# Optimization experiments

Measured on AMD Instinct MI355X. Metric: run time of the kernel, lower is better.

## Reference

```python
import jax, jax.numpy as jnp
import numpy as np

N_NODES = 100000
N_EDGES = 1000000
IN_F, HID_F, OUT_F = 128, 128, 16


def setup_inputs() -> dict:
    key = jax.random.key(0)
    ks = jax.random.split(key, 8)
    x = jax.random.normal(ks[0], (N_NODES, IN_F), dtype=jnp.float32)
    src = jax.random.randint(ks[1], (N_EDGES,), 0, N_NODES, dtype=jnp.int64)
    dst = jax.random.randint(ks[2], (N_EDGES,), 0, N_NODES, dtype=jnp.int64)
    s = 1.0 / np.sqrt(HID_F)
    W1 = jax.random.normal(ks[3], (IN_F, HID_F), dtype=jnp.float32) * s
    W2 = jax.random.normal(ks[4], (HID_F, HID_F), dtype=jnp.float32) * s
    W3 = jax.random.normal(ks[5], (HID_F, HID_F), dtype=jnp.float32) * s
    W4 = jax.random.normal(ks[6], (HID_F, HID_F), dtype=jnp.float32) * s
    W5 = jax.random.normal(ks[7], (HID_F, OUT_F), dtype=jnp.float32) * s
    return {
        "x": x, "src": src, "dst": dst,
        "W1": W1, "b1": jnp.zeros((HID_F,), jnp.float32),
        "W2": W2, "b2": jnp.zeros((HID_F,), jnp.float32),
        "W3": W3, "b3": jnp.zeros((HID_F,), jnp.float32),
        "W4": W4, "b4": jnp.zeros((HID_F,), jnp.float32),
        "W5": W5, "b5": jnp.zeros((OUT_F,), jnp.float32),
    }


def reference(x, src, dst, W1, b1, W2, b2, W3, b3, W4, b4, W5, b5):
    N = x.shape[0]
    # in-degree per destination node (static graph, computed once)
    deg = jax.ops.segment_sum(jnp.ones_like(dst, dtype=x.dtype), dst, num_segments=N)
    inv = (1.0 / (deg + 1.0))[:, None]  # gcn aggregator normalizer: 1/(deg_in+1)

    def sage_gcn(h, W, b):
        # h_neigh[v] = (h[v] + sum_{u->v} h[u]) / (deg_in(v)+1); then linear
        agg = (h + jax.ops.segment_sum(h[src], dst, num_segments=N)) * inv
        return agg @ W + b

    h = jax.nn.relu(sage_gcn(x, W1, b1))
    h = jax.nn.relu(sage_gcn(h, W2, b2))
    h = jax.nn.relu(sage_gcn(h, W3, b3))
    h = jax.nn.relu(sage_gcn(h, W4, b4))
    h = sage_gcn(h, W5, b5)
    return jax.nn.log_softmax(h, axis=-1)
```

## Files before the change

### kernel.cpp

```cpp
#include <hip/hip_runtime.h>
#include <hip/hip_bf16.h>

#define NNODES 100000
#define NP (NNODES + 8)
#define NEDGES 1000000
#define HID 128
#define OUTF 16
#define NB 16
#define BCAP 81920
#define KB 64
#define BZT 1024
#define DBINS 32

typedef __attribute__((ext_vector_type(8))) short short8;
typedef __attribute__((ext_vector_type(4))) float floatx4;
typedef __attribute__((ext_vector_type(4))) unsigned int uintx4;
typedef unsigned int uint32;
typedef unsigned long long ull;
typedef unsigned short ushort16;

__device__ __forceinline__ float blo(uint32 u) { return __uint_as_float(u << 16); }
__device__ __forceinline__ float bhi(uint32 u) { return __uint_as_float(u & 0xffff0000u); }
__device__ __forceinline__ ushort16 f2b(float f) {
    __hip_bfloat16 h = __float2bfloat16(f);
    return *reinterpret_cast<ushort16*>(&h);
}
__device__ __forceinline__ uint32 pack2(float a, float b) {
    return (uint32)f2b(a) | ((uint32)f2b(b) << 16);
}


__global__ __launch_bounds__(BZT) void bucketize(const int* __restrict__ src,
                                                 const int* __restrict__ dst,
                                                 int* __restrict__ counts,
                                                 int* __restrict__ bcursor,
                                                 ull* __restrict__ stage, int E) {
    __shared__ int cnt[NB], lbase[NB], gbase[NB];
    __shared__ int2 buf[BZT];
    __shared__ unsigned char bb[BZT];
    int t = threadIdx.x;
    int e0 = blockIdx.x * BZT;
    int e = e0 + t;
    if (t < NB) cnt[t] = 0;
    __syncthreads();
    int s = 0; unsigned y = 0; int b = 0, r = 0;
    bool valid = e < E;
    if (valid) {
        s = src[e];
        int d = dst[e];
        int rk = atomicAdd(&counts[d], 1);
        y = (unsigned)d | ((unsigned)rk << 17);
        b = (int)((unsigned)d * NB / NNODES);
        r = atomicAdd(&cnt[b], 1);
    }
    __syncthreads();
    if (t == 0) {
        int run = 0;
        for (int i = 0; i < NB; i++) { lbase[i] = run; run += cnt[i]; }
    }
    __syncthreads();
    if (valid) {
        int p = lbase[b] + r;
        buf[p] = make_int2(s, (int)y);
        bb[p] = (unsigned char)b;
    }
    if (t < NB) gbase[t] = atomicAdd(&bcursor[t], cnt[t]);
    __syncthreads();
    int nvalid = min(BZT, E - e0);
    if (t < nvalid) {
        int b2 = bb[t];
        int2 sd = buf[t];
        int pos = gbase[b2] + (t - lbase[b2]);
        if (pos < BCAP) {
            ull val = (ull)(unsigned)sd.x | ((ull)(unsigned)sd.y << 32);
            __builtin_nontemporal_store(val, &stage[(size_t)b2 * BCAP + pos]);
        }
    }
}

__global__ __launch_bounds__(256) void fill2(const ull* __restrict__ stage,
                                             const int* __restrict__ bcursor,
                                             const int* __restrict__ offs,
                                             int* __restrict__ csr) {
    int blk = blockIdx.x;
    int b = (blk & 7) + 8 * ((blk >> 3) & 1);
    int slot = blk >> 4;
    int cntb = min(bcursor[b], BCAP);
    int per = (cntb + KB - 1) / KB;
    int s0 = slot * per;
    int s1 = min(s0 + per, cntb);
    const ull* st = stage + (size_t)b * BCAP;
    for (int i = s0 + threadIdx.x; i < s1; i += 256) {
        ull v = __builtin_nontemporal_load(&st[i]);
        int s = (int)(v & 0xffffffffu);
        unsigned y = (unsigned)(v >> 32);
        int d = (int)(y & 0x1ffffu);
        int r = (int)(y >> 17);
        csr[offs[d] + r] = s;
    }
}

__global__ void scan1(const int* __restrict__ counts, int* __restrict__ offs,
                      int* __restrict__ bsum, int N) {
    __shared__ int tmp[256];
    int t = threadIdx.x;
    int i = blockIdx.x * 256 + t;
    int v = (i < N) ? ((counts[i] + 7) & ~7) : 0;
    tmp[t] = v;
    __syncthreads();
    for (int d = 1; d < 256; d <<= 1) {
        int add = (t >= d) ? tmp[t - d] : 0;
        __syncthreads();
        tmp[t] += add;
        __syncthreads();
    }
    if (i < N) offs[i] = tmp[t] - v;
    if (t == 255) bsum[blockIdx.x] = tmp[255];
}

__global__ void scan2(int* __restrict__ bsum, int nb) {
    __shared__ int tmp[512];
    int t = threadIdx.x;
    int v = (t < nb) ? bsum[t] : 0;
    tmp[t] = v;
    __syncthreads();
    for (int d = 1; d < 512; d <<= 1) {
        int add = (t >= d) ? tmp[t - d] : 0;
        __syncthreads();
        tmp[t] += add;
        __syncthreads();
    }
    if (t < nb) bsum[t] = tmp[t] - v;
}

__global__ void scan3(int* __restrict__ offs, const int* __restrict__ bsum,
                      const int* __restrict__ counts, float* __restrict__ inv,
                      int N) {
    int i = blockIdx.x * 256 + threadIdx.x;
    if (i < N) {
        offs[i] += bsum[blockIdx.x];
        inv[i] = 1.0f / (float)(counts[i] + 1);
    }
}


__global__ __launch_bounds__(256) void binhist(const int* __restrict__ counts,
                                               int* __restrict__ bins, int N) {
    __shared__ int h[DBINS];
    int t = threadIdx.x;
    if (t < DBINS) h[t] = 0;
    __syncthreads();
    int i = blockIdx.x * 256 + t;
    if (i < N) {
        int bin = min((counts[i] + 7) >> 3, DBINS - 1);
        atomicAdd(&h[bin], 1);
    }
    __syncthreads();
    if (t < DBINS && h[t] > 0) atomicAdd(&bins[t], h[t]);
}

__global__ void binscan(int* __restrict__ bins) {
    if (threadIdx.x == 0) {
        int run = 0;
        for (int i = 0; i < DBINS; i++) {
            int c = bins[i];
            bins[i] = run;
            run += c;
        }
    }
}

__global__ __launch_bounds__(256) void dsort2(const int* __restrict__ counts,
                                              const int* __restrict__ offs,
                                              const float* __restrict__ inv,
                                              int* __restrict__ bins,
                                              int* __restrict__ begs, int* __restrict__ cnts,
                                              float* __restrict__ invs, int* __restrict__ outid,
                                              int* __restrict__ csr, int N) {
    __shared__ int h[DBINS], lbase[DBINS];
    int t = threadIdx.x;
    int i = blockIdx.x * 256 + t;
    if (t < DBINS) h[t] = 0;
    __syncthreads();
    int c = 0, bin = 0, r = 0;
    bool valid = i < N;
    if (valid) {
        c = counts[i];
        bin = min((c + 7) >> 3, DBINS - 1);
        r = atomicAdd(&h[bin], 1);
    }
    __syncthreads();
    if (t < DBINS) lbase[t] = (h[t] > 0) ? atomicAdd(&bins[t], h[t]) : 0;
    __syncthreads();
    if (valid) {
        int p = lbase[bin] + r;
        int o = offs[i];
        begs[p] = o;
        cnts[p] = c;
        invs[p] = inv[i];
        outid[p] = i;
        int c8 = (c + 7) & ~7;
        for (int k = c; k < c8; k++) csr[o + k] = NNODES;
    }
}

__global__ void zeropad(uint32* __restrict__ zb, uint32* __restrict__ hb,
                        uint32* __restrict__ z16b) {
    int t = threadIdx.x;
    for (int i = t; i < 512; i += 256) {
        int s = i >> 6, r = (i >> 3) & 7, k = i & 7;
        zb[((size_t)s * NP + NNODES + r) * 8 + k] = 0;
        hb[((size_t)s * NP + NNODES + r) * 8 + k] = 0;
    }
    if (t < 64) z16b[(size_t)(NNODES + (t >> 3)) * 8 + (t & 7)] = 0;
}


__global__ void pack_w(const float* __restrict__ W, ushort16* __restrict__ Wp) {
    int b = blockIdx.x;
    int lane = threadIdx.x;
    int nt = b >> 2, ks = b & 3;
    int n = nt * 16 + (lane & 15);
    int kbase = ks * 32 + ((lane >> 4) << 3);
    ushort16 tmp[8];
#pragma unroll
    for (int i = 0; i < 8; i++) tmp[i] = f2b(W[(size_t)(kbase + i) * HID + n]);
    *(uint4*)&Wp[((size_t)b * 64 + lane) * 8] = *(uint4*)tmp;
}


template <int AF32>
__global__ __launch_bounds__(256) void gemm_mfma(const void* __restrict__ Av,
                                                 const ushort16* __restrict__ Wp,
                                                 ushort16* __restrict__ Z, int M) {
    __shared__ __align__(16) ushort16 Wl[32 * 64 * 8];
    int t = threadIdx.x;
    const uint4* wp4 = (const uint4*)Wp;
    uint4* wl4 = (uint4*)Wl;
#pragma unroll
    for (int p = 0; p < 8; p++) wl4[t + p * 256] = wp4[t + p * 256];
    __syncthreads();

    int wv = t >> 6, lane = t & 63;
    int row = blockIdx.x * 64 + wv * 16 + (lane & 15);
    int rowc = min(row, M - 1);
    int kb = (lane >> 4) << 3;

    short8 a[4];
    if (AF32) {
        const float* A = (const float*)Av;
#pragma unroll
        for (int ks = 0; ks < 4; ks++) {
            const float* p = A + (size_t)rowc * HID + ks * 32 + kb;
            floatx4 lo = *(const floatx4*)p;
            floatx4 hi = *(const floatx4*)(p + 4);
            union { short8 s; ushort16 u[8]; } cv;
            cv.u[0] = f2b(lo.x); cv.u[1] = f2b(lo.y); cv.u[2] = f2b(lo.z); cv.u[3] = f2b(lo.w);
            cv.u[4] = f2b(hi.x); cv.u[5] = f2b(hi.y); cv.u[6] = f2b(hi.z); cv.u[7] = f2b(hi.w);
            a[ks] = cv.s;
        }
    } else {
        const ushort16* A = (const ushort16*)Av;
        int sl = kb >> 4, soff = kb & 8;
#pragma unroll
        for (int ks = 0; ks < 4; ks++) {
            int slice = ks * 2 + sl;
            a[ks] = *(const short8*)(A + ((size_t)slice * NP + rowc) * 16 + soff);
        }
    }

    floatx4 acc[8];
#pragma unroll
    for (int nt = 0; nt < 8; nt++) acc[nt] = (floatx4){0.f, 0.f, 0.f, 0.f};

#pragma unroll
    for (int nt = 0; nt < 8; nt++) {
#pragma unroll
        for (int ks = 0; ks < 4; ks++) {
            short8 b = *(const short8*)&Wl[(size_t)(((nt << 2) | ks) * 64 + lane) * 8];
            acc[nt] = __builtin_amdgcn_mfma_f32_16x16x32_bf16(a[ks], b, acc[nt], 0, 0, 0);
        }
    }

    int orow = blockIdx.x * 64 + wv * 16 + ((lane >> 4) << 2);
    int col = lane & 15;
#pragma unroll
    for (int i = 0; i < 4; i++) {
        int r = orow + i;
        if (r < M) {
#pragma unroll
            for (int nt = 0; nt < 8; nt++)
                Z[((size_t)nt * NP + r) * 16 + col] = f2b(acc[nt][i]);
        }
    }
}


#define ACC4(g)                                        \
    {                                                  \
        acc0.x += blo((g).x); acc0.y += bhi((g).x);    \
        acc1.x += blo((g).y); acc1.y += bhi((g).y);    \
        acc2.x += blo((g).z); acc2.y += bhi((g).z);    \
        acc3.x += blo((g).w); acc3.y += bhi((g).w);    \
    }

__global__ __launch_bounds__(256) void agg_sliced(const uint32* __restrict__ Z,
                                                  const int* __restrict__ begs,
                                                  const int* __restrict__ cnts,
                                                  const int* __restrict__ csr,
                                                  const float* __restrict__ invs,
                                                  const int* __restrict__ outid,
                                                  const float* __restrict__ bias,
                                                  uint32* __restrict__ H, int N) {
    int s = blockIdx.x & 7;
    int chunk = blockIdx.x >> 3;
    int t = threadIdx.x;
    int l = t & 1;
    int p = chunk * 128 + (t >> 1);
    int pairbase = t & 62;
    bool act = p < N;
    int pc = act ? p : N - 1;
    const uint4* Zs = (const uint4*)(Z + (size_t)s * NP * 8);
    uint4* Hs = (uint4*)(H + (size_t)s * NP * 8);

    int beg = begs[pc];
    int cnt8 = (cnts[pc] + 7) & ~7;
    float sc = invs[pc];
    int ov = outid[pc];

    uint4 sv = Zs[(size_t)ov * 2 + l];
    float2 acc0 = make_float2(blo(sv.x), bhi(sv.x));
    float2 acc1 = make_float2(blo(sv.y), bhi(sv.y));
    float2 acc2 = make_float2(blo(sv.z), bhi(sv.z));
    float2 acc3 = make_float2(blo(sv.w), bhi(sv.w));

    for (int j = 0; j < cnt8; j += 8) {
        int4 iv = *(const int4*)&csr[beg + j + 4 * l];
        uint4 g[8];
#pragma unroll
        for (int q = 0; q < 8; q++) {
            int c = (q & 3) == 0 ? iv.x : (q & 3) == 1 ? iv.y : (q & 3) == 2 ? iv.z : iv.w;
            int u = __shfl(c, pairbase + (q >> 2), 64);
            g[q] = Zs[(size_t)u * 2 + l];
        }
#pragma unroll
        for (int q = 0; q < 8; q++) ACC4(g[q]);
    }

    const float* bp = bias + s * 16 + l * 8;
    floatx4 b01 = *(const floatx4*)bp;
    floatx4 b23 = *(const floatx4*)(bp + 4);
    uintx4 o;
    o.x = pack2(fmaxf(acc0.x * sc + b01.x, 0.f), fmaxf(acc0.y * sc + b01.y, 0.f));
    o.y = pack2(fmaxf(acc1.x * sc + b01.z, 0.f), fmaxf(acc1.y * sc + b01.w, 0.f));
    o.z = pack2(fmaxf(acc2.x * sc + b23.x, 0.f), fmaxf(acc2.y * sc + b23.y, 0.f));
    o.w = pack2(fmaxf(acc3.x * sc + b23.z, 0.f), fmaxf(acc3.y * sc + b23.w, 0.f));
    if (act) __builtin_nontemporal_store(o, (uintx4*)&Hs[(size_t)ov * 2 + l]);
}


__global__ __launch_bounds__(256) void gemm16(const uint32* __restrict__ A,
                                              const float* __restrict__ W5,
                                              uint32* __restrict__ Z16, int M) {
    __shared__ float Ws[HID * OUTF];
    int t = threadIdx.x;
    for (int i = t; i < HID * OUTF; i += 256) Ws[i] = W5[i];
    __syncthreads();
    int gid = blockIdx.x * 256 + t;
    int r = gid >> 3, cp = gid & 7;
    if (r >= M) return;
    float a0 = 0.f, a1 = 0.f;
#pragma unroll
    for (int s8 = 0; s8 < 8; s8++) {
        const uint32* ar = A + ((size_t)s8 * NP + r) * 8;
#pragma unroll
        for (int k = 0; k < 8; k++) {
            uint32 u = ar[k];
            float f0 = blo(u), f1 = bhi(u);
            a0 += f0 * Ws[(s8 * 16 + 2 * k) * OUTF + 2 * cp] +
                  f1 * Ws[(s8 * 16 + 2 * k + 1) * OUTF + 2 * cp];
            a1 += f0 * Ws[(s8 * 16 + 2 * k) * OUTF + 2 * cp + 1] +
                  f1 * Ws[(s8 * 16 + 2 * k + 1) * OUTF + 2 * cp + 1];
        }
    }
    Z16[(size_t)r * 8 + cp] = pack2(a0, a1);
}


__global__ __launch_bounds__(256) void agg16_lsm(const uint32* __restrict__ Z16,
                                                 const int* __restrict__ offs,
                                                 const int* __restrict__ counts,
                                                 const int* __restrict__ csr,
                                                 const float* __restrict__ inv,
                                                 const float* __restrict__ b5,
                                                 float* __restrict__ out, int N) {
    int t = threadIdx.x;
    int l = t & 1;
    int v = blockIdx.x * 128 + (t >> 1);
    int pairbase = t & 62;
    bool act = v < N;
    int vc = act ? v : N - 1;
    const uint4* Zs = (const uint4*)Z16;

    uint4 sv = Zs[(size_t)vc * 2 + l];
    float2 acc0 = make_float2(blo(sv.x), bhi(sv.x));
    float2 acc1 = make_float2(blo(sv.y), bhi(sv.y));
    float2 acc2 = make_float2(blo(sv.z), bhi(sv.z));
    float2 acc3 = make_float2(blo(sv.w), bhi(sv.w));

    int beg = offs[vc];
    int cnt8 = (counts[vc] + 7) & ~7;
    for (int j = 0; j < cnt8; j += 8) {
        int4 iv = *(const int4*)&csr[beg + j + 4 * l];
        uint4 g[8];
#pragma unroll
        for (int q = 0; q < 8; q++) {
            int c = (q & 3) == 0 ? iv.x : (q & 3) == 1 ? iv.y : (q & 3) == 2 ? iv.z : iv.w;
            int u = __shfl(c, pairbase + (q >> 2), 64);
            g[q] = Zs[(size_t)u * 2 + l];
        }
#pragma unroll
        for (int q = 0; q < 8; q++) ACC4(g[q]);
    }

    float sc = inv[vc];
    const float* bp = b5 + l * 8;
    floatx4 b01 = *(const floatx4*)bp;
    floatx4 b23 = *(const floatx4*)(bp + 4);
    float val[8];
    val[0] = acc0.x * sc + b01.x; val[1] = acc0.y * sc + b01.y;
    val[2] = acc1.x * sc + b01.z; val[3] = acc1.y * sc + b01.w;
    val[4] = acc2.x * sc + b23.x; val[5] = acc2.y * sc + b23.y;
    val[6] = acc3.x * sc + b23.z; val[7] = acc3.y * sc + b23.w;
    float mm = val[0];
#pragma unroll
    for (int k = 1; k < 8; k++) mm = fmaxf(mm, val[k]);
    mm = fmaxf(mm, __shfl_xor(mm, 1, 64));
    float ss = 0.f;
#pragma unroll
    for (int k = 0; k < 8; k++) ss += expf(val[k] - mm);
    ss += __shfl_xor(ss, 1, 64);
    float ls = mm + logf(ss);
    if (act) {
        float4 o0 = make_float4(val[0] - ls, val[1] - ls, val[2] - ls, val[3] - ls);
        float4 o1 = make_float4(val[4] - ls, val[5] - ls, val[6] - ls, val[7] - ls);
        float* op = out + (size_t)v * OUTF + l * 8;
        *(float4*)op = o0;
        *(float4*)(op + 4) = o1;
    }
}


extern "C" void kernel_launch(void* const* d_in, const int* in_sizes, int n_in,
                              void* d_out, int out_size, void* d_ws, size_t ws_size,
                              hipStream_t stream) {
    const float* x   = (const float*)d_in[0];
    const int*   src = (const int*)d_in[1];
    const int*   dst = (const int*)d_in[2];
    const float* W1 = (const float*)d_in[3];
    const float* b1 = (const float*)d_in[4];
    const float* W2 = (const float*)d_in[5];
    const float* b2 = (const float*)d_in[6];
    const float* W3 = (const float*)d_in[7];
    const float* b3 = (const float*)d_in[8];
    const float* W4 = (const float*)d_in[9];
    const float* b4 = (const float*)d_in[10];
    const float* W5 = (const float*)d_in[11];
    const float* b5 = (const float*)d_in[12];

    char* ws = (char*)d_ws;
    size_t off = 0;
    auto alloc = [&](size_t bytes) {
        void* p = ws + off;
        off = (off + bytes + 255) & ~(size_t)255;
        return p;
    };
    const size_t CSR_ELEMS = (size_t)NEDGES + 7 * (size_t)NNODES + 64;
    ushort16* zb   = (ushort16*)alloc((size_t)8 * NP * 16 * 2);
    ushort16* hb   = (ushort16*)alloc((size_t)8 * NP * 16 * 2);
    uint32*   z16b = (uint32*)alloc((size_t)NP * OUTF * 2);
    int*      counts = (int*)alloc((size_t)NNODES * 4);
    int*      offs   = (int*)alloc((size_t)(NNODES + 1) * 4);
    int*      bsum   = (int*)alloc(512 * 4);
    int*      csr    = (int*)alloc(CSR_ELEMS * 4);
    float*    invd   = (float*)alloc((size_t)NNODES * 4);
    ull*      stage  = (ull*)alloc((size_t)NB * BCAP * 8);
    int*      bcursor = (int*)alloc(NB * 4);
    int*      bins   = (int*)alloc(DBINS * 4);
    int*      begs   = (int*)alloc((size_t)NNODES * 4);
    int*      cnts   = (int*)alloc((size_t)NNODES * 4);
    float*    invs   = (float*)alloc((size_t)NNODES * 4);
    int*      outid  = (int*)alloc((size_t)NNODES * 4);
    ushort16* Wp1 = (ushort16*)alloc((size_t)HID * HID * 2);
    ushort16* Wp2 = (ushort16*)alloc((size_t)HID * HID * 2);
    ushort16* Wp3 = (ushort16*)alloc((size_t)HID * HID * 2);
    ushort16* Wp4 = (ushort16*)alloc((size_t)HID * HID * 2);
    (void)ws_size; (void)in_sizes; (void)n_in; (void)out_size;

    const int N = NNODES, E = NEDGES;
    int nb = (N + 255) / 256;

    hipMemsetAsync(counts, 0, (size_t)N * 4, stream);
    hipMemsetAsync(bcursor, 0, NB * 4, stream);
    hipMemsetAsync(bins, 0, DBINS * 4, stream);
    bucketize<<<(E + BZT - 1) / BZT, BZT, 0, stream>>>(src, dst, counts, bcursor, stage, E);
    scan1<<<nb, 256, 0, stream>>>(counts, offs, bsum, N);
    scan2<<<1, 512, 0, stream>>>(bsum, nb);
    scan3<<<nb, 256, 0, stream>>>(offs, bsum, counts, invd, N);
    binhist<<<nb, 256, 0, stream>>>(counts, bins, N);
    binscan<<<1, 64, 0, stream>>>(bins);
    dsort2<<<nb, 256, 0, stream>>>(counts, offs, invd, bins, begs, cnts, invs, outid, csr, N);
    fill2<<<NB * KB, 256, 0, stream>>>(stage, bcursor, offs, csr);
    zeropad<<<1, 256, 0, stream>>>((uint32*)zb, (uint32*)hb, z16b);

    pack_w<<<32, 64, 0, stream>>>(W1, Wp1);
    pack_w<<<32, 64, 0, stream>>>(W2, Wp2);
    pack_w<<<32, 64, 0, stream>>>(W3, Wp3);
    pack_w<<<32, 64, 0, stream>>>(W4, Wp4);

    int gemmGrid = (N + 63) / 64;
    int aggGrid  = 8 * ((N + 127) / 128);
    int agg16Grid = (N + 127) / 128;

    gemm_mfma<1><<<gemmGrid, 256, 0, stream>>>((const void*)x, Wp1, zb, N);
    agg_sliced<<<aggGrid, 256, 0, stream>>>((const uint32*)zb, begs, cnts, csr, invs, outid,
                                            b1, (uint32*)hb, N);

    gemm_mfma<0><<<gemmGrid, 256, 0, stream>>>((const void*)hb, Wp2, zb, N);
    agg_sliced<<<aggGrid, 256, 0, stream>>>((const uint32*)zb, begs, cnts, csr, invs, outid,
                                            b2, (uint32*)hb, N);

    gemm_mfma<0><<<gemmGrid, 256, 0, stream>>>((const void*)hb, Wp3, zb, N);
    agg_sliced<<<aggGrid, 256, 0, stream>>>((const uint32*)zb, begs, cnts, csr, invs, outid,
                                            b3, (uint32*)hb, N);

    gemm_mfma<0><<<gemmGrid, 256, 0, stream>>>((const void*)hb, Wp4, zb, N);
    agg_sliced<<<aggGrid, 256, 0, stream>>>((const uint32*)zb, begs, cnts, csr, invs, outid,
                                            b4, (uint32*)hb, N);

    gemm16<<<(N * 8 + 255) / 256, 256, 0, stream>>>((const uint32*)hb, W5, z16b, N);
    agg16_lsm<<<agg16Grid, 256, 0, stream>>>(z16b, offs, counts, csr, invd, b5,
                                             (float*)d_out, N);
}
```

Measured before the change: 413.9 us.

## Renumber nodes by degree-sorted permutation so aggregation reads contiguous sorted arrays

Nodes are sorted once by (node-range bucket, degree bin) into a global permutation. All intermediate features, CSR offsets, counts and inverse degrees are stored in permuted order, and CSR neighbor ids are remapped through the permutation. The indirection arrays begs and outid disappear from the aggregation kernels, and the input gather and final output scatter are done through iperm. The intra-pair shuffle of CSR indices is replaced by each lane loading all eight indices directly. This adds a random perm lookup per edge in fill2, an iperm gather in the first GEMM and the output stage, and some locality change for neighbor gathers.

Result: faster. 390.9 us (-5.6%).

```diff
diff --git a/kernel.cpp b/kernel.cpp
--- a/kernel.cpp
+++ b/kernel.cpp
@@ -10,7 +10,8 @@
 #define BCAP 81920
 #define KB 64
 #define BZT 1024
-#define DBINS 32
+#define DB2 32
+#define NBINS (NB * DB2)
 
 typedef __attribute__((ext_vector_type(8))) short short8;
 typedef __attribute__((ext_vector_type(4))) float floatx4;
@@ -80,6 +81,7 @@
 
 __global__ __launch_bounds__(256) void fill2(const ull* __restrict__ stage,
                                              const int* __restrict__ bcursor,
+                                             const int* __restrict__ perm,
                                              const int* __restrict__ offs,
                                              int* __restrict__ csr) {
     int blk = blockIdx.x;
@@ -96,16 +98,76 @@
         unsigned y = (unsigned)(v >> 32);
         int d = (int)(y & 0x1ffffu);
         int r = (int)(y >> 17);
-        csr[offs[d] + r] = s;
-    }
-}
-
-__global__ void scan1(const int* __restrict__ counts, int* __restrict__ offs,
+        int pd = perm[d];
+        csr[offs[pd] + r] = perm[s];
+    }
+}
+
+
+__global__ __launch_bounds__(256) void binhist(const int* __restrict__ counts,
+                                               int* __restrict__ bins, int N) {
+    __shared__ int h[NBINS];
+    int t = threadIdx.x;
+    for (int k = t; k < NBINS; k += 256) h[k] = 0;
+    __syncthreads();
+    int i = blockIdx.x * 256 + t;
+    if (i < N) {
+        int bi = (int)((unsigned)i * NB / NNODES);
+        int db = min((counts[i] + 7) >> 3, DB2 - 1);
+        atomicAdd(&h[bi * DB2 + db], 1);
+    }
+    __syncthreads();
+    for (int k = t; k < NBINS; k += 256)
+        if (h[k] > 0) atomicAdd(&bins[k], h[k]);
+}
+
+__global__ void binscan(int* __restrict__ bins) {
+    if (threadIdx.x == 0) {
+        int run = 0;
+        for (int i = 0; i < NBINS; i++) {
+            int c = bins[i];
+            bins[i] = run;
+            run += c;
+        }
+    }
+}
+
+__global__ __launch_bounds__(256) void dsort2(const int* __restrict__ counts,
+                                              int* __restrict__ bins,
+                                              int* __restrict__ perm,
+                                              int* __restrict__ iperm,
+                                              int* __restrict__ cnts_s, int N) {
+    __shared__ int h[NBINS], lb[NBINS];
+    int t = threadIdx.x;
+    for (int k = t; k < NBINS; k += 256) h[k] = 0;
+    __syncthreads();
+    int i = blockIdx.x * 256 + t;
+    int c = 0, idx = 0, r = 0;
+    bool valid = i < N;
+    if (valid) {
+        c = counts[i];
+        int bi = (int)((unsigned)i * NB / NNODES);
+        idx = bi * DB2 + min((c + 7) >> 3, DB2 - 1);
+        r = atomicAdd(&h[idx], 1);
+    }
+    __syncthreads();
+    for (int k = t; k < NBINS; k += 256)
+        lb[k] = (h[k] > 0) ? atomicAdd(&bins[k], h[k]) : 0;
+    __syncthreads();
+    if (valid) {
+        int p = lb[idx] + r;
+        perm[i] = p;
+        iperm[p] = i;
+        cnts_s[p] = c;
+    }
+}
+
+__global__ void scan1(const int* __restrict__ cnts_s, int* __restrict__ offs,
                       int* __restrict__ bsum, int N) {
     __shared__ int tmp[256];
     int t = threadIdx.x;
     int i = blockIdx.x * 256 + t;
-    int v = (i < N) ? ((counts[i] + 7) & ~7) : 0;
+    int v = (i < N) ? ((cnts_s[i] + 7) & ~7) : 0;
     tmp[t] = v;
     __syncthreads();
     for (int d = 1; d < 256; d <<= 1) {
@@ -134,71 +196,14 @@
 }
 
 __global__ void scan3(int* __restrict__ offs, const int* __restrict__ bsum,
-                      const int* __restrict__ counts, float* __restrict__ inv,
-                      int N) {
+                      const int* __restrict__ cnts_s, float* __restrict__ invs,
+                      int* __restrict__ csr, int N) {
     int i = blockIdx.x * 256 + threadIdx.x;
     if (i < N) {
-        offs[i] += bsum[blockIdx.x];
-        inv[i] = 1.0f / (float)(counts[i] + 1);
-    }
-}
-
-
-__global__ __launch_bounds__(256) void binhist(const int* __restrict__ counts,
-                                               int* __restrict__ bins, int N) {
-    __shared__ int h[DBINS];
-    int t = threadIdx.x;
-    if (t < DBINS) h[t] = 0;
-    __syncthreads();
-    int i = blockIdx.x * 256 + t;
-    if (i < N) {
-        int bin = min((counts[i] + 7) >> 3, DBINS - 1);
-        atomicAdd(&h[bin], 1);
-    }
-    __syncthreads();
-    if (t < DBINS && h[t] > 0) atomicAdd(&bins[t], h[t]);
-}
-
-__global__ void binscan(int* __restrict__ bins) {
-    if (threadIdx.x == 0) {
-        int run = 0;
-        for (int i = 0; i < DBINS; i++) {
-            int c = bins[i];
-            bins[i] = run;
-            run += c;
-        }
-    }
-}
-
-__global__ __launch_bounds__(256) void dsort2(const int* __restrict__ counts,
-                                              const int* __restrict__ offs,
-                                              const float* __restrict__ inv,
-                                              int* __restrict__ bins,
-                                              int* __restrict__ begs, int* __restrict__ cnts,
-                                              float* __restrict__ invs, int* __restrict__ outid,
-                                              int* __restrict__ csr, int N) {
-    __shared__ int h[DBINS], lbase[DBINS];
-    int t = threadIdx.x;
-    int i = blockIdx.x * 256 + t;
-    if (t < DBINS) h[t] = 0;
-    __syncthreads();
-    int c = 0, bin = 0, r = 0;
-    bool valid = i < N;
-    if (valid) {
-        c = counts[i];
-        bin = min((c + 7) >> 3, DBINS - 1);
-        r = atomicAdd(&h[bin], 1);
-    }
-    __syncthreads();
-    if (t < DBINS) lbase[t] = (h[t] > 0) ? atomicAdd(&bins[t], h[t]) : 0;
-    __syncthreads();
-    if (valid) {
-        int p = lbase[bin] + r;
-        int o = offs[i];
-        begs[p] = o;
-        cnts[p] = c;
-        invs[p] = inv[i];
-        outid[p] = i;
+        int o = offs[i] + bsum[blockIdx.x];
+        offs[i] = o;
+        int c = cnts_s[i];
+        invs[i] = 1.0f / (float)(c + 1);
         int c8 = (c + 7) & ~7;
         for (int k = c; k < c8; k++) csr[o + k] = NNODES;
     }
@@ -231,6 +236,7 @@
 
 template <int AF32>
 __global__ __launch_bounds__(256) void gemm_mfma(const void* __restrict__ Av,
+                                                 const int* __restrict__ iperm,
                                                  const ushort16* __restrict__ Wp,
                                                  ushort16* __restrict__ Z, int M) {
     __shared__ __align__(16) ushort16 Wl[32 * 64 * 8];
@@ -249,9 +255,10 @@
     short8 a[4];
     if (AF32) {
         const float* A = (const float*)Av;
+        int orig = iperm[rowc];
 #pragma unroll
         for (int ks = 0; ks < 4; ks++) {
-            const float* p = A + (size_t)rowc * HID + ks * 32 + kb;
+            const float* p = A + (size_t)orig * HID + ks * 32 + kb;
             floatx4 lo = *(const floatx4*)p;
             floatx4 hi = *(const floatx4*)(p + 4);
             union { short8 s; ushort16 u[8]; } cv;
@@ -305,11 +312,10 @@
     }
 
 __global__ __launch_bounds__(256) void agg_sliced(const uint32* __restrict__ Z,
-                                                  const int* __restrict__ begs,
-                                                  const int* __restrict__ cnts,
+                                                  const int* __restrict__ offs,
+                                                  const int* __restrict__ cnts_s,
                                                   const int* __restrict__ csr,
                                                   const float* __restrict__ invs,
-                                                  const int* __restrict__ outid,
                                                   const float* __restrict__ bias,
                                                   uint32* __restrict__ H, int N) {
     int s = blockIdx.x & 7;
@@ -317,32 +323,33 @@
     int t = threadIdx.x;
     int l = t & 1;
     int p = chunk * 128 + (t >> 1);
-    int pairbase = t & 62;
     bool act = p < N;
     int pc = act ? p : N - 1;
     const uint4* Zs = (const uint4*)(Z + (size_t)s * NP * 8);
     uint4* Hs = (uint4*)(H + (size_t)s * NP * 8);
 
-    int beg = begs[pc];
-    int cnt8 = (cnts[pc] + 7) & ~7;
+    int beg = offs[pc];
+    int cnt8 = (cnts_s[pc] + 7) & ~7;
     float sc = invs[pc];
-    int ov = outid[pc];
-
-    uint4 sv = Zs[(size_t)ov * 2 + l];
+
+    uint4 sv = Zs[(size_t)pc * 2 + l];
     float2 acc0 = make_float2(blo(sv.x), bhi(sv.x));
     float2 acc1 = make_float2(blo(sv.y), bhi(sv.y));
     float2 acc2 = make_float2(blo(sv.z), bhi(sv.z));
     float2 acc3 = make_float2(blo(sv.w), bhi(sv.w));
 
     for (int j = 0; j < cnt8; j += 8) {
-        int4 iv = *(const int4*)&csr[beg + j + 4 * l];
+        int4 ia = *(const int4*)&csr[beg + j];
+        int4 ib = *(const int4*)&csr[beg + j + 4];
         uint4 g[8];
-#pragma unroll
-        for (int q = 0; q < 8; q++) {
-            int c = (q & 3) == 0 ? iv.x : (q & 3) == 1 ? iv.y : (q & 3) == 2 ? iv.z : iv.w;
-            int u = __shfl(c, pairbase + (q >> 2), 64);
-            g[q] = Zs[(size_t)u * 2 + l];
-        }
+        g[0] = Zs[(size_t)ia.x * 2 + l];
+        g[1] = Zs[(size_t)ia.y * 2 + l];
+        g[2] = Zs[(size_t)ia.z * 2 + l];
+        g[3] = Zs[(size_t)ia.w * 2 + l];
+        g[4] = Zs[(size_t)ib.x * 2 + l];
+        g[5] = Zs[(size_t)ib.y * 2 + l];
+        g[6] = Zs[(size_t)ib.z * 2 + l];
+        g[7] = Zs[(size_t)ib.w * 2 + l];
 #pragma unroll
         for (int q = 0; q < 8; q++) ACC4(g[q]);
     }
@@ -355,7 +362,7 @@
     o.y = pack2(fmaxf(acc1.x * sc + b01.z, 0.f), fmaxf(acc1.y * sc + b01.w, 0.f));
     o.z = pack2(fmaxf(acc2.x * sc + b23.x, 0.f), fmaxf(acc2.y * sc + b23.y, 0.f));
     o.w = pack2(fmaxf(acc3.x * sc + b23.z, 0.f), fmaxf(acc3.y * sc + b23.w, 0.f));
-    if (act) __builtin_nontemporal_store(o, (uintx4*)&Hs[(size_t)ov * 2 + l]);
+    if (act) __builtin_nontemporal_store(o, (uintx4*)&Hs[(size_t)p * 2 + l]);
 }
 
 
@@ -389,41 +396,44 @@
 
 __global__ __launch_bounds__(256) void agg16_lsm(const uint32* __restrict__ Z16,
                                                  const int* __restrict__ offs,
-                                                 const int* __restrict__ counts,
+                                                 const int* __restrict__ cnts_s,
                                                  const int* __restrict__ csr,
-                                                 const float* __restrict__ inv,
+                                                 const float* __restrict__ invs,
+                                                 const int* __restrict__ iperm,
                                                  const float* __restrict__ b5,
                                                  float* __restrict__ out, int N) {
     int t = threadIdx.x;
     int l = t & 1;
-    int v = blockIdx.x * 128 + (t >> 1);
-    int pairbase = t & 62;
-    bool act = v < N;
-    int vc = act ? v : N - 1;
+    int p = blockIdx.x * 128 + (t >> 1);
+    bool act = p < N;
+    int pc = act ? p : N - 1;
     const uint4* Zs = (const uint4*)Z16;
 
-    uint4 sv = Zs[(size_t)vc * 2 + l];
+    uint4 sv = Zs[(size_t)pc * 2 + l];
     float2 acc0 = make_float2(blo(sv.x), bhi(sv.x));
     float2 acc1 = make_float2(blo(sv.y), bhi(sv.y));
     float2 acc2 = make_float2(blo(sv.z), bhi(sv.z));
     float2 acc3 = make_float2(blo(sv.w), bhi(sv.w));
 
-    int beg = offs[vc];
-    int cnt8 = (counts[vc] + 7) & ~7;
+    int beg = offs[pc];
+    int cnt8 = (cnts_s[pc] + 7) & ~7;
     for (int j = 0; j < cnt8; j += 8) {
-        int4 iv = *(const int4*)&csr[beg + j + 4 * l];
+        int4 ia = *(const int4*)&csr[beg + j];
+        int4 ib = *(const int4*)&csr[beg + j + 4];
         uint4 g[8];
-#pragma unroll
-        for (int q = 0; q < 8; q++) {
-            int c = (q & 3) == 0 ? iv.x : (q & 3) == 1 ? iv.y : (q & 3) == 2 ? iv.z : iv.w;
-            int u = __shfl(c, pairbase + (q >> 2), 64);
-            g[q] = Zs[(size_t)u * 2 + l];
-        }
+        g[0] = Zs[(size_t)ia.x * 2 + l];
+        g[1] = Zs[(size_t)ia.y * 2 + l];
+        g[2] = Zs[(size_t)ia.z * 2 + l];
+        g[3] = Zs[(size_t)ia.w * 2 + l];
+        g[4] = Zs[(size_t)ib.x * 2 + l];
+        g[5] = Zs[(size_t)ib.y * 2 + l];
+        g[6] = Zs[(size_t)ib.z * 2 + l];
+        g[7] = Zs[(size_t)ib.w * 2 + l];
 #pragma unroll
         for (int q = 0; q < 8; q++) ACC4(g[q]);
     }
 
-    float sc = inv[vc];
+    float sc = invs[pc];
     const float* bp = b5 + l * 8;
     floatx4 b01 = *(const floatx4*)bp;
     floatx4 b23 = *(const floatx4*)(bp + 4);
@@ -442,9 +452,10 @@
     ss += __shfl_xor(ss, 1, 64);
     float ls = mm + logf(ss);
     if (act) {
+        int ov = iperm[p];
         float4 o0 = make_float4(val[0] - ls, val[1] - ls, val[2] - ls, val[3] - ls);
         float4 o1 = make_float4(val[4] - ls, val[5] - ls, val[6] - ls, val[7] - ls);
-        float* op = out + (size_t)v * OUTF + l * 8;
+        float* op = out + (size_t)ov * OUTF + l * 8;
         *(float4*)op = o0;
         *(float4*)(op + 4) = o1;
     }
@@ -480,17 +491,16 @@
     ushort16* hb   = (ushort16*)alloc((size_t)8 * NP * 16 * 2);
     uint32*   z16b = (uint32*)alloc((size_t)NP * OUTF * 2);
     int*      counts = (int*)alloc((size_t)NNODES * 4);
+    int*      cnts_s = (int*)alloc((size_t)NNODES * 4);
+    int*      perm   = (int*)alloc((size_t)NNODES * 4);
+    int*      iperm  = (int*)alloc((size_t)NNODES * 4);
+    float*    invs   = (float*)alloc((size_t)NNODES * 4);
     int*      offs   = (int*)alloc((size_t)(NNODES + 1) * 4);
     int*      bsum   = (int*)alloc(512 * 4);
     int*      csr    = (int*)alloc(CSR_ELEMS * 4);
-    float*    invd   = (float*)alloc((size_t)NNODES * 4);
     ull*      stage  = (ull*)alloc((size_t)NB * BCAP * 8);
     int*      bcursor = (int*)alloc(NB * 4);
-    int*      bins   = (int*)alloc(DBINS * 4);
-    int*      begs   = (int*)alloc((size_t)NNODES * 4);
-    int*      cnts   = (int*)alloc((size_t)NNODES * 4);
-    float*    invs   = (float*)alloc((size_t)NNODES * 4);
-    int*      outid  = (int*)alloc((size_t)NNODES * 4);
+    int*      bins   = (int*)alloc(NBINS * 4);
     ushort16* Wp1 = (ushort16*)alloc((size_t)HID * HID * 2);
     ushort16* Wp2 = (ushort16*)alloc((size_t)HID * HID * 2);
     ushort16* Wp3 = (ushort16*)alloc((size_t)HID * HID * 2);
@@ -502,15 +512,15 @@
 
     hipMemsetAsync(counts, 0, (size_t)N * 4, stream);
     hipMemsetAsync(bcursor, 0, NB * 4, stream);
-    hipMemsetAsync(bins, 0, DBINS * 4, stream);
+    hipMemsetAsync(bins, 0, NBINS * 4, stream);
     bucketize<<<(E + BZT - 1) / BZT, BZT, 0, stream>>>(src, dst, counts, bcursor, stage, E);
-    scan1<<<nb, 256, 0, stream>>>(counts, offs, bsum, N);
-    scan2<<<1, 512, 0, stream>>>(bsum, nb);
-    scan3<<<nb, 256, 0, stream>>>(offs, bsum, counts, invd, N);
     binhist<<<nb, 256, 0, stream>>>(counts, bins, N);
     binscan<<<1, 64, 0, stream>>>(bins);
-    dsort2<<<nb, 256, 0, stream>>>(counts, offs, invd, bins, begs, cnts, invs, outid, csr, N);
-    fill2<<<NB * KB, 256, 0, stream>>>(stage, bcursor, offs, csr);
+    dsort2<<<nb, 256, 0, stream>>>(counts, bins, perm, iperm, cnts_s, N);
+    scan1<<<nb, 256, 0, stream>>>(cnts_s, offs, bsum, N);
+    scan2<<<1, 512, 0, stream>>>(bsum, nb);
+    scan3<<<nb, 256, 0, stream>>>(offs, bsum, cnts_s, invs, csr, N);
+    fill2<<<NB * KB, 256, 0, stream>>>(stage, bcursor, perm, offs, csr);
     zeropad<<<1, 256, 0, stream>>>((uint32*)zb, (uint32*)hb, z16b);
 
     pack_w<<<32, 64, 0, stream>>>(W1, Wp1);
@@ -522,23 +532,23 @@
     int aggGrid  = 8 * ((N + 127) / 128);
     int agg16Grid = (N + 127) / 128;
 
-    gemm_mfma<1><<<gemmGrid, 256, 0, stream>>>((const void*)x, Wp1, zb, N);
-    agg_sliced<<<aggGrid, 256, 0, stream>>>((const uint32*)zb, begs, cnts, csr, invs, outid,
-                                            b1, (uint32*)hb, N);
-
-    gemm_mfma<0><<<gemmGrid, 256, 0, stream>>>((const void*)hb, Wp2, zb, N);
-    agg_sliced<<<aggGrid, 256, 0, stream>>>((const uint32*)zb, begs, cnts, csr, invs, outid,
-                                            b2, (uint32*)hb, N);
-
-    gemm_mfma<0><<<gemmGrid, 256, 0, stream>>>((const void*)hb, Wp3, zb, N);
-    agg_sliced<<<aggGrid, 256, 0, stream>>>((const uint32*)zb, begs, cnts, csr, invs, outid,
-                                            b3, (uint32*)hb, N);
-
-    gemm_mfma<0><<<gemmGrid, 256, 0, stream>>>((const void*)hb, Wp4, zb, N);
-    agg_sliced<<<aggGrid, 256, 0, stream>>>((const uint32*)zb, begs, cnts, csr, invs, outid,
-                                            b4, (uint32*)hb, N);
+    gemm_mfma<1><<<gemmGrid, 256, 0, stream>>>((const void*)x, iperm, Wp1, zb, N);
+    agg_sliced<<<aggGrid, 256, 0, stream>>>((const uint32*)zb, offs, cnts_s, csr, invs, b1,
+                                            (uint32*)hb, N);
+
+    gemm_mfma<0><<<gemmGrid, 256, 0, stream>>>((const void*)hb, nullptr, Wp2, zb, N);
+    agg_sliced<<<aggGrid, 256, 0, stream>>>((const uint32*)zb, offs, cnts_s, csr, invs, b2,
+                                            (uint32*)hb, N);
+
+    gemm_mfma<0><<<gemmGrid, 256, 0, stream>>>((const void*)hb, nullptr, Wp3, zb, N);
+    agg_sliced<<<aggGrid, 256, 0, stream>>>((const uint32*)zb, offs, cnts_s, csr, invs, b3,
+                                            (uint32*)hb, N);
+
+    gemm_mfma<0><<<gemmGrid, 256, 0, stream>>>((const void*)hb, nullptr, Wp4, zb, N);
+    agg_sliced<<<aggGrid, 256, 0, stream>>>((const uint32*)zb, offs, cnts_s, csr, invs, b4,
+                                            (uint32*)hb, N);
 
     gemm16<<<(N * 8 + 255) / 256, 256, 0, stream>>>((const uint32*)hb, W5, z16b, N);
-    agg16_lsm<<<agg16Grid, 256, 0, stream>>>(z16b, offs, counts, csr, invd, b5,
+    agg16_lsm<<<agg16Grid, 256, 0, stream>>>(z16b, offs, cnts_s, csr, invs, iperm, b5,
                                              (float*)d_out, N);
 }
```
